# Performance work log

Hardware: AMD Instinct MI355X
Metric: run time of the kernel (lower is better)

Reference implementation:

```python
import jax, jax.numpy as jnp
import numpy as np

B, T, C = 2, 2048, 2048
H, KV = 16, 4
D = C // H            # 128 head dim
G = H // KV           # 4 query heads per kv head
THETA = 10000.0


def setup_inputs() -> dict:
    key = jax.random.key(0)
    k0, k1, k2, k3 = jax.random.split(key, 4)
    s = 1.0 / np.sqrt(C)
    return {
        "x": jax.random.normal(k0, (B, T, C), jnp.float32),
        "Wq": jax.random.normal(k1, (H * D, C), jnp.float32) * s,
        "Wkv": jax.random.normal(k2, (2 * KV * D, C), jnp.float32) * s,
        "Wo": jax.random.normal(k3, (C, C), jnp.float32) * s,
    }


def _rotate_half(x):
    d = x.shape[-1] // 2
    return jnp.concatenate([-x[..., d:], x[..., :d]], axis=-1)


def _rope_tables(t, d):
    freqs = 1.0 / (THETA ** (jnp.arange(0, d, 2, dtype=jnp.float32) / d))
    ang = jnp.arange(t, dtype=jnp.float32)[:, None] * freqs[None, :]  # [T, d/2]
    emb = jnp.concatenate([ang, ang], axis=-1)                         # [T, d]
    return jnp.cos(emb), jnp.sin(emb)


def reference(x, Wq, Wkv, Wo):
    b, t, c = x.shape
    q = (x @ Wq.T).reshape(b, t, H, D).transpose(0, 2, 1, 3)      # [B,H,T,D]
    kv = (x @ Wkv.T).reshape(b, t, 2 * KV, D)
    k = kv[:, :, :KV].transpose(0, 2, 1, 3)                        # [B,KV,T,D]
    v = kv[:, :, KV:].transpose(0, 2, 1, 3)                        # [B,KV,T,D]

    cos, sin = _rope_tables(t, D)
    cos, sin = cos[None, None], sin[None, None]                    # [1,1,T,D]
    q = q * cos + _rotate_half(q) * sin
    k = k * cos + _rotate_half(k) * sin

    # GQA: keep k/v at KV heads; reshape q into [B,KV,G,T,D] instead of expanding k/v.
    qg = q.reshape(b, KV, G, t, D)
    scores = jnp.einsum('bkgtd,bksd->bkgts', qg, k) / jnp.sqrt(jnp.float32(D))
    causal = jnp.tril(jnp.ones((t, t), dtype=bool))                # is_causal=True path
    scores = jnp.where(causal, scores, -jnp.inf)
    p = jax.nn.softmax(scores, axis=-1)
    y = jnp.einsum('bkgts,bksd->bkgtd', p, v)                      # [B,KV,G,T,D]
    y = y.reshape(b, H, t, D).transpose(0, 2, 1, 3).reshape(b, t, c)
    return y @ Wo.T
```

## Files before the change

### kernel.cpp

```cpp
#include <hip/hip_runtime.h>

typedef unsigned short u16;
typedef __attribute__((ext_vector_type(4))) float f32x4;
typedef __attribute__((ext_vector_type(8))) __bf16 bf16x8;

__device__ __forceinline__ u16 f2bf(float f) {
    unsigned int x = __float_as_uint(f);
    x += 0x7fffu + ((x >> 16) & 1u);
    return (u16)(x >> 16);
}
__device__ __forceinline__ float bf2f(u16 u) {
    return __uint_as_float(((unsigned int)u) << 16);
}
__device__ __forceinline__ void async16(const void* g, void* l) {
    __builtin_amdgcn_global_load_lds(
        (const __attribute__((address_space(1))) void*)g,
        (__attribute__((address_space(3))) void*)l,
        16, 0, 0);
}
__device__ __forceinline__ void barrier_fence() {
    asm volatile("" ::: "memory");
    __builtin_amdgcn_s_barrier();
    asm volatile("" ::: "memory");
}

__global__ __launch_bounds__(256)
void cvt_all(const float* __restrict__ x,  const float* __restrict__ wq,
             const float* __restrict__ wkv, const float* __restrict__ wo,
             u16* __restrict__ xb, u16* __restrict__ wqb,
             u16* __restrict__ wkvb, u16* __restrict__ wob)
{
    const int nx = 8388608, nq = 4194304, nkv = 2097152;
    const int i = (blockIdx.x * 256 + threadIdx.x) * 4;
    const float* src; u16* dst; int off;
    if (i < nx)                 { src = x;   dst = xb;   off = i; }
    else if (i < nx + nq)       { src = wq;  dst = wqb;  off = i - nx; }
    else if (i < nx + nq + nkv) { src = wkv; dst = wkvb; off = i - nx - nq; }
    else                        { src = wo;  dst = wob;  off = i - nx - nq - nkv; }
    const float4 v = *(const float4*)(src + off);
    ushort4 o;
    o.x = f2bf(v.x); o.y = f2bf(v.y); o.z = f2bf(v.z); o.w = f2bf(v.w);
    *(ushort4*)(dst + off) = o;
}

__global__ __launch_bounds__(256, 3)
void gemm_qkv(const u16* __restrict__ A,
              const u16* __restrict__ B0,
              const u16* __restrict__ B1,
              u16* __restrict__ C,
              u16* __restrict__ vbuf,
              int M, int K)
{
    constexpr int ASZ = 128 * 32;
    __shared__ __align__(16) u16 As[3 * ASZ];
    __shared__ __align__(16) u16 Bs[3 * ASZ];

    const int tid  = threadIdx.x;
    const int w    = tid >> 6;
    const int lane = tid & 63;
    const int fl   = lane & 15;
    const int q4   = lane >> 4;
    const int wm   = w >> 1;
    const int wn   = w & 1;

    const int gx  = gridDim.x;
    const int nwg = gx * gridDim.y;
    int id = blockIdx.y * gx + blockIdx.x;
    id = (id & 7) * (nwg >> 3) + (id >> 3);
    const int m0 = (id / gx) * 128;
    const int n0 = (id % gx) * 128;

    const u16* Bp = B0;
    int nb = n0;
    if (n0 >= 2048) { Bp = B1; nb = n0 - 2048; }

    const int srow = w * 16 + (lane >> 2);
    const int sg   = (lane & 3) ^ ((lane >> 3) & 3);
    const u16* agp = A  + (size_t)(m0 + srow) * K + sg * 8;
    const u16* bgp = Bp + (size_t)(nb + srow) * K + sg * 8;
    const int sLds = w * 512;

    const int cSlot = (q4 ^ ((fl >> 1) & 3)) * 8;

    f32x4 acc[4][4];
    #pragma unroll
    for (int i = 0; i < 4; ++i)
        #pragma unroll
        for (int j = 0; j < 4; ++j)
            acc[i][j] = f32x4{0.f, 0.f, 0.f, 0.f};

    const int NT = K >> 5;

    auto stage = [&](int t, int bf) {
        const size_t kof = (size_t)t * 32;
        async16(agp + kof,                   &As[bf * ASZ + sLds]);
        async16(agp + (size_t)64 * K + kof,  &As[bf * ASZ + 2048 + sLds]);
        async16(bgp + kof,                   &Bs[bf * ASZ + sLds]);
        async16(bgp + (size_t)64 * K + kof,  &Bs[bf * ASZ + 2048 + sLds]);
    };

    stage(0, 0);
    stage(1, 1);

    int bf = 0;
    for (int t = 0; t < NT; ++t) {
        if (t < NT - 1) asm volatile("s_waitcnt vmcnt(4)" ::: "memory");
        else            asm volatile("s_waitcnt vmcnt(0)" ::: "memory");
        barrier_fence();
        const int bf2 = (bf + 2 >= 3) ? bf - 1 : bf + 2;
        if (t + 2 < NT) stage(t + 2, bf2);

        const int ab = bf * ASZ + (wm * 64 + fl) * 32 + cSlot;
        const int bb = bf * ASZ + (wn * 32 + fl) * 32 + cSlot;
        bf16x8 a[4], b[4];
        #pragma unroll
        for (int mt = 0; mt < 4; ++mt)
            a[mt] = *(const bf16x8*)&As[ab + mt * 512];
        b[0] = *(const bf16x8*)&Bs[bb];
        b[1] = *(const bf16x8*)&Bs[bb + 512];
        b[2] = *(const bf16x8*)&Bs[bb + 2048];
        b[3] = *(const bf16x8*)&Bs[bb + 2560];

        #pragma unroll
        for (int mt = 0; mt < 4; ++mt)
            #pragma unroll
            for (int nt = 0; nt < 4; ++nt)
                acc[mt][nt] = __builtin_amdgcn_mfma_f32_16x16x32_bf16(
                    a[mt], b[nt], acc[mt][nt], 0, 0, 0);

        bf = (bf + 1 >= 3) ? 0 : bf + 1;
    }

    if (n0 < 2560) {
        const float sc = (n0 < 2048) ? 0.08838834764831845f : 1.0f;
        float inv[2];
        #pragma unroll
        for (int j = 0; j < 2; ++j)
            inv[j] = exp2f(-(float)(wn * 32 + j * 16 + fl) * 0.2076205f);
        #pragma unroll
        for (int mt = 0; mt < 4; ++mt) {
            #pragma unroll
            for (int r = 0; r < 4; ++r) {
                const int row = m0 + wm * 64 + mt * 16 + q4 * 4 + r;
                const float pos = (float)(row & 2047);
                #pragma unroll
                for (int j = 0; j < 2; ++j) {
                    float s, c;
                    __sincosf(pos * inv[j], &s, &c);
                    const float x1 = acc[mt][j][r];
                    const float x2 = acc[mt][j + 2][r];
                    const int i0 = wn * 32 + j * 16 + fl;
                    C[(size_t)row * 3072 + n0 + i0]      = f2bf((x1 * c - x2 * s) * sc);
                    C[(size_t)row * 3072 + n0 + 64 + i0] = f2bf((x2 * c + x1 * s) * sc);
                }
            }
        }
    } else {
        #pragma unroll
        for (int mt = 0; mt < 4; ++mt)
            #pragma unroll
            for (int j = 0; j < 4; ++j) {
                const int colb = n0 + wn * 32 + (j & 1) * 16 + (j >> 1) * 64 + fl;
                const int f = colb - 2560;
                #pragma unroll
                for (int r = 0; r < 4; ++r) {
                    const int row = m0 + wm * 64 + mt * 16 + q4 * 4 + r;
                    const int tt = row & 2047;
                    const int bb2 = row >> 11;
                    vbuf[((size_t)((bb2 << 2) + (f >> 7)) * 128 + (f & 127)) * 2048 + tt] =
                        f2bf(acc[mt][j][r]);
                }
            }
    }
}

__global__ __launch_bounds__(256, 3)
void gemm128r(const u16* __restrict__ A,
              const u16* __restrict__ B0,
              float* __restrict__ Cf,
              int M, int N, int K)
{
    constexpr int ASZ = 128 * 32;
    __shared__ __align__(16) u16 As[3 * ASZ];
    __shared__ __align__(16) u16 Bs[3 * ASZ];

    const int tid  = threadIdx.x;
    const int w    = tid >> 6;
    const int lane = tid & 63;
    const int fl   = lane & 15;
    const int q4   = lane >> 4;
    const int wm   = w >> 1;
    const int wn   = w & 1;

    const int gx  = gridDim.x;
    const int nwg = gx * gridDim.y;
    int id = blockIdx.y * gx + blockIdx.x;
    id = (id & 7) * (nwg >> 3) + (id >> 3);
    const int m0 = (id / gx) * 128;
    const int n0 = (id % gx) * 128;

    const int srow = w * 16 + (lane >> 2);
    const int sg   = (lane & 3) ^ ((lane >> 3) & 3);
    const u16* agp = A  + (size_t)(m0 + srow) * K + sg * 8;
    const u16* bgp = B0 + (size_t)(n0 + srow) * K + sg * 8;
    const int sLds = w * 512;

    const int cSlot = (q4 ^ ((fl >> 1) & 3)) * 8;

    f32x4 acc[4][4];
    #pragma unroll
    for (int i = 0; i < 4; ++i)
        #pragma unroll
        for (int j = 0; j < 4; ++j)
            acc[i][j] = f32x4{0.f, 0.f, 0.f, 0.f};

    const int NT = K >> 5;

    auto stage = [&](int t, int bf) {
        const size_t kof = (size_t)t * 32;
        async16(agp + kof,                   &As[bf * ASZ + sLds]);
        async16(agp + (size_t)64 * K + kof,  &As[bf * ASZ + 2048 + sLds]);
        async16(bgp + kof,                   &Bs[bf * ASZ + sLds]);
        async16(bgp + (size_t)64 * K + kof,  &Bs[bf * ASZ + 2048 + sLds]);
    };

    stage(0, 0);
    stage(1, 1);

    int bf = 0;
    for (int t = 0; t < NT; ++t) {
        if (t < NT - 1) asm volatile("s_waitcnt vmcnt(4)" ::: "memory");
        else            asm volatile("s_waitcnt vmcnt(0)" ::: "memory");
        barrier_fence();
        const int bf2 = (bf + 2 >= 3) ? bf - 1 : bf + 2;
        if (t + 2 < NT) stage(t + 2, bf2);

        const int ab = bf * ASZ + (wm * 64 + fl) * 32 + cSlot;
        const int bb = bf * ASZ + (wn * 64 + fl) * 32 + cSlot;
        bf16x8 a[4], b[4];
        #pragma unroll
        for (int mt = 0; mt < 4; ++mt)
            a[mt] = *(const bf16x8*)&As[ab + mt * 512];
        #pragma unroll
        for (int nt = 0; nt < 4; ++nt)
            b[nt] = *(const bf16x8*)&Bs[bb + nt * 512];

        #pragma unroll
        for (int mt = 0; mt < 4; ++mt)
            #pragma unroll
            for (int nt = 0; nt < 4; ++nt)
                acc[mt][nt] = __builtin_amdgcn_mfma_f32_16x16x32_bf16(
                    a[mt], b[nt], acc[mt][nt], 0, 0, 0);

        bf = (bf + 1 >= 3) ? 0 : bf + 1;
    }

    #pragma unroll
    for (int mt = 0; mt < 4; ++mt)
        #pragma unroll
        for (int nt = 0; nt < 4; ++nt) {
            const int colb = n0 + wn * 64 + nt * 16 + fl;
            #pragma unroll
            for (int r = 0; r < 4; ++r) {
                const int row = m0 + wm * 64 + mt * 16 + q4 * 4 + r;
                Cf[(size_t)row * N + colb] = acc[mt][nt][r];
            }
        }
}

__global__ __launch_bounds__(256, 2)
void attn_kernel(const u16* __restrict__ qkv,
                 const u16* __restrict__ vsrc,
                 u16* __restrict__ y)
{
    constexpr int T = 2048;
    const int lo  = blockIdx.x;
    const int hi  = 31 - lo;
    const int bh  = blockIdx.y;
    const int b   = bh >> 4;
    const int h   = bh & 15;
    const int kvh = h >> 2;

    const int tid  = threadIdx.x;
    const int w    = tid >> 6;
    const int lane = tid & 63;
    const int fl   = lane & 15;
    const int q4   = lane >> 4;

    __shared__ __align__(16) u16 Ks[2][64 * 128];
    __shared__ __align__(16) u16 Vt[2][128 * 64];
    __shared__ __align__(16) u16 Ps[64 * 72];

    const u16* Qg = qkv  + (size_t)(b * T) * 3072 + (h << 7);
    const u16* Kg = qkv  + (size_t)(b * T) * 3072 + 2048 + (kvh << 7);
    const u16* Vg = vsrc + (size_t)((b * 4 + kvh) * 128) * T;

    bf16x8 qf0[4], qf1[4];
    #pragma unroll
    for (int kc = 0; kc < 4; ++kc) {
        qf0[kc] = *(const bf16x8*)&Qg[(size_t)(lo * 64 + w * 16 + fl) * 3072 + kc * 32 + q4 * 8];
        qf1[kc] = *(const bf16x8*)&Qg[(size_t)(hi * 64 + w * 16 + fl) * 3072 + kc * 32 + q4 * 8];
    }

    int goffK[4], goffV[4], ldsC[4];
    #pragma unroll
    for (int i = 0; i < 4; ++i) {
        const int c  = w + 4 * i;
        const int rk = 4 * c + (lane >> 4);
        const int lk = (lane & 15) ^ (rk & 15);
        goffK[i] = rk * 3072 + lk * 8;
        const int rv = 8 * c + (lane >> 3);
        const int lv = (lane & 7) ^ ((lane >> 3) & 7);
        goffV[i] = rv * T + lv * 8;
        ldsC[i]  = c * 512;
    }

    #pragma unroll
    for (int i = 0; i < 4; ++i) {
        async16(Kg + goffK[i], &Ks[0][ldsC[i]]);
        async16(Vg + goffV[i], &Vt[0][ldsC[i]]);
    }

    float l0 = 0.f, l1 = 0.f;
    f32x4 o0[8], o1[8];
    #pragma unroll
    for (int dt = 0; dt < 8; ++dt) {
        o0[dt] = f32x4{0.f, 0.f, 0.f, 0.f};
        o1[dt] = f32x4{0.f, 0.f, 0.f, 0.f};
    }

    const int psrow = (w * 16 + fl) * 72;

    for (int j = 0; j <= hi; ++j) {
        __syncthreads();

        if (j < hi) {
            const u16* kb = Kg + (size_t)(j + 1) * 64 * 3072;
            const u16* vb = Vg + (j + 1) * 64;
            const int nb = (j + 1) & 1;
            #pragma unroll
            for (int i = 0; i < 4; ++i) {
                async16(kb + goffK[i], &Ks[nb][ldsC[i]]);
                async16(vb + goffV[i], &Vt[nb][ldsC[i]]);
            }
        }
        const int cb = j & 1;
        const bool dual = (j <= lo);

        f32x4 s0[4], s1[4];
        #pragma unroll
        for (int nt = 0; nt < 4; ++nt) {
            s0[nt] = f32x4{0.f, 0.f, 0.f, 0.f};
            s1[nt] = f32x4{0.f, 0.f, 0.f, 0.f};
        }
        if (dual) {
            #pragma unroll
            for (int kc = 0; kc < 4; ++kc)
                #pragma unroll
                for (int nt = 0; nt < 4; ++nt) {
                    bf16x8 aK = *(const bf16x8*)
                        &Ks[cb][(nt * 16 + fl) * 128 + (((kc << 2) + q4) ^ fl) * 8];
                    s1[nt] = __builtin_amdgcn_mfma_f32_16x16x32_bf16(aK, qf1[kc], s1[nt], 0, 0, 0);
                    s0[nt] = __builtin_amdgcn_mfma_f32_16x16x32_bf16(aK, qf0[kc], s0[nt], 0, 0, 0);
                }
        } else {
            #pragma unroll
            for (int kc = 0; kc < 4; ++kc)
                #pragma unroll
                for (int nt = 0; nt < 4; ++nt) {
                    bf16x8 aK = *(const bf16x8*)
                        &Ks[cb][(nt * 16 + fl) * 128 + (((kc << 2) + q4) ^ fl) * 8];
                    s1[nt] = __builtin_amdgcn_mfma_f32_16x16x32_bf16(aK, qf1[kc], s1[nt], 0, 0, 0);
                }
        }

        if (j == lo || j == hi) {
            const int qloc = w * 16 + fl;
            #pragma unroll
            for (int nt = 0; nt < 4; ++nt)
                #pragma unroll
                for (int r = 0; r < 4; ++r)
                    if (nt * 16 + q4 * 4 + r > qloc) {
                        if (j == lo) s0[nt][r] = -3e38f;
                        else         s1[nt][r] = -3e38f;
                    }
        }

        if (dual) {
            #pragma unroll
            for (int nt = 0; nt < 4; ++nt) {
                ushort4 pw;
                float p0 = __expf(s0[nt][0]);
                float p1 = __expf(s0[nt][1]);
                float p2 = __expf(s0[nt][2]);
                float p3 = __expf(s0[nt][3]);
                l0 += (p0 + p1) + (p2 + p3);
                pw.x = f2bf(p0); pw.y = f2bf(p1); pw.z = f2bf(p2); pw.w = f2bf(p3);
                *(ushort4*)&Ps[psrow + nt * 16 + q4 * 4] = pw;
            }
            asm volatile("s_waitcnt lgkmcnt(0)" ::: "memory");
            #pragma unroll
            for (int kc = 0; kc < 2; ++kc) {
                bf16x8 ap = *(const bf16x8*)&Ps[psrow + kc * 32 + q4 * 8];
                #pragma unroll
                for (int dt = 0; dt < 8; ++dt) {
                    bf16x8 bv = *(const bf16x8*)
                        &Vt[cb][(dt * 16 + fl) * 64 + (((kc << 2) + q4) ^ (fl & 7)) * 8];
                    o0[dt] = __builtin_amdgcn_mfma_f32_16x16x32_bf16(ap, bv, o0[dt], 0, 0, 0);
                }
            }
        }

        #pragma unroll
        for (int nt = 0; nt < 4; ++nt) {
            ushort4 pw;
            float p0 = __expf(s1[nt][0]);
            float p1 = __expf(s1[nt][1]);
            float p2 = __expf(s1[nt][2]);
            float p3 = __expf(s1[nt][3]);
            l1 += (p0 + p1) + (p2 + p3);
            pw.x = f2bf(p0); pw.y = f2bf(p1); pw.z = f2bf(p2); pw.w = f2bf(p3);
            *(ushort4*)&Ps[psrow + nt * 16 + q4 * 4] = pw;
        }
        asm volatile("s_waitcnt lgkmcnt(0)" ::: "memory");
        #pragma unroll
        for (int kc = 0; kc < 2; ++kc) {
            bf16x8 ap = *(const bf16x8*)&Ps[psrow + kc * 32 + q4 * 8];
            #pragma unroll
            for (int dt = 0; dt < 8; ++dt) {
                bf16x8 bv = *(const bf16x8*)
                    &Vt[cb][(dt * 16 + fl) * 64 + (((kc << 2) + q4) ^ (fl & 7)) * 8];
                o1[dt] = __builtin_amdgcn_mfma_f32_16x16x32_bf16(ap, bv, o1[dt], 0, 0, 0);
            }
        }
    }

    l0 += __shfl_xor(l0, 16, 64);
    l0 += __shfl_xor(l0, 32, 64);
    l1 += __shfl_xor(l1, 16, 64);
    l1 += __shfl_xor(l1, 32, 64);
    const float li0 = 1.0f / l0;
    const float li1 = 1.0f / l1;

    float lr0[4], lr1[4];
    #pragma unroll
    for (int r = 0; r < 4; ++r) {
        lr0[r] = __shfl(li0, q4 * 4 + r, 16);
        lr1[r] = __shfl(li1, q4 * 4 + r, 16);
    }
    #pragma unroll
    for (int dt = 0; dt < 8; ++dt)
        #pragma unroll
        for (int r = 0; r < 4; ++r) {
            const int row0 = lo * 64 + w * 16 + q4 * 4 + r;
            const int row1 = hi * 64 + w * 16 + q4 * 4 + r;
            y[(size_t)(b * T + row0) * 2048 + (h << 7) + dt * 16 + fl] =
                f2bf(o0[dt][r] * lr0[r]);
            y[(size_t)(b * T + row1) * 2048 + (h << 7) + dt * 16 + fl] =
                f2bf(o1[dt][r] * lr1[r]);
        }
}

extern "C" void kernel_launch(void* const* d_in, const int* in_sizes, int n_in,
                              void* d_out, int out_size, void* d_ws, size_t ws_size,
                              hipStream_t stream)
{
    const float* x   = (const float*)d_in[0];
    const float* Wq  = (const float*)d_in[1];
    const float* Wkv = (const float*)d_in[2];
    const float* Wo  = (const float*)d_in[3];
    float* out = (float*)d_out;

    const int nx = 4096 * 2048, nq = 2048 * 2048, nkv = 1024 * 2048, no = 2048 * 2048;

    u16* xb   = (u16*)d_ws;
    u16* wqb  = xb  + nx;
    u16* wkvb = wqb + nq;
    u16* wob  = wkvb + nkv;
    u16* qkv  = wob + no;
    u16* vbuf = qkv + (size_t)4096 * 3072;
    u16* y    = vbuf + (size_t)2 * 4 * 128 * 2048;

    const int ntot = nx + nq + nkv + no;
    cvt_all<<<ntot / 1024, 256, 0, stream>>>(x, Wq, Wkv, Wo, xb, wqb, wkvb, wob);

    dim3 g1(3072 / 128, 4096 / 128);
    gemm_qkv<<<g1, 256, 0, stream>>>(xb, wqb, wkvb, qkv, vbuf, 4096, 2048);

    attn_kernel<<<dim3(16, 32), 256, 0, stream>>>(qkv, vbuf, y);

    dim3 g2(2048 / 128, 4096 / 128);
    gemm128r<<<g2, 256, 0, stream>>>(y, wob, out, 4096, 2048, 2048);
}
```

Before: 273.3 us.

## Rework attention around 32x32 MFMA with register-resident P

```diff
diff --git a/kernel.cpp b/kernel.cpp
--- a/kernel.cpp
+++ b/kernel.cpp
@@ -2,6 +2,7 @@
 
 typedef unsigned short u16;
 typedef __attribute__((ext_vector_type(4))) float f32x4;
+typedef __attribute__((ext_vector_type(16))) float f32x16;
 typedef __attribute__((ext_vector_type(8))) __bf16 bf16x8;
 
 __device__ __forceinline__ u16 f2bf(float f) {
@@ -22,6 +23,11 @@
     asm volatile("" ::: "memory");
     __builtin_amdgcn_s_barrier();
     asm volatile("" ::: "memory");
+}
+__device__ __forceinline__ unsigned cvtpk(float lo, float hi) {
+    unsigned d;
+    asm("v_cvt_pk_bf16_f32 %0, %1, %2" : "=v"(d) : "v"(lo), "v"(hi));
+    return d;
 }
 
 __global__ __launch_bounds__(256)
@@ -274,191 +280,135 @@
                  u16* __restrict__ y)
 {
     constexpr int T = 2048;
-    const int lo  = blockIdx.x;
-    const int hi  = 31 - lo;
-    const int bh  = blockIdx.y;
-    const int b   = bh >> 4;
-    const int h   = bh & 15;
-    const int kvh = h >> 2;
+    const int bh = blockIdx.x;
+    const int by = blockIdx.y;
+    const int qt = (by < 8) ? by : 23 - by;
+    const int b = bh >> 4, h = bh & 15, kvh = h >> 2;
 
     const int tid  = threadIdx.x;
     const int w    = tid >> 6;
     const int lane = tid & 63;
-    const int fl   = lane & 15;
-    const int q4   = lane >> 4;
-
-    __shared__ __align__(16) u16 Ks[2][64 * 128];
-    __shared__ __align__(16) u16 Vt[2][128 * 64];
-    __shared__ __align__(16) u16 Ps[64 * 72];
+    const int l31  = lane & 31;
+    const int hh   = lane >> 5;
+
+    __shared__ __align__(16) u16 Ks[2][32 * 128];
+    __shared__ __align__(16) u16 Vt[2][128 * 32];
 
     const u16* Qg = qkv  + (size_t)(b * T) * 3072 + (h << 7);
     const u16* Kg = qkv  + (size_t)(b * T) * 3072 + 2048 + (kvh << 7);
     const u16* Vg = vsrc + (size_t)((b * 4 + kvh) * 128) * T;
 
-    bf16x8 qf0[4], qf1[4];
-    #pragma unroll
-    for (int kc = 0; kc < 4; ++kc) {
-        qf0[kc] = *(const bf16x8*)&Qg[(size_t)(lo * 64 + w * 16 + fl) * 3072 + kc * 32 + q4 * 8];
-        qf1[kc] = *(const bf16x8*)&Qg[(size_t)(hi * 64 + w * 16 + fl) * 3072 + kc * 32 + q4 * 8];
-    }
-
-    int goffK[4], goffV[4], ldsC[4];
-    #pragma unroll
-    for (int i = 0; i < 4; ++i) {
+    const int qb = qt * 128 + w * 32;
+    bf16x8 qf[8];
+    #pragma unroll
+    for (int kc = 0; kc < 8; ++kc)
+        qf[kc] = *(const bf16x8*)&Qg[(size_t)(qb + l31) * 3072 + kc * 16 + hh * 8];
+
+    int goffK[2], goffV[2], ldsC[2];
+    #pragma unroll
+    for (int i = 0; i < 2; ++i) {
         const int c  = w + 4 * i;
         const int rk = 4 * c + (lane >> 4);
         const int lk = (lane & 15) ^ (rk & 15);
         goffK[i] = rk * 3072 + lk * 8;
-        const int rv = 8 * c + (lane >> 3);
-        const int lv = (lane & 7) ^ ((lane >> 3) & 7);
+        const int rv = 16 * c + (lane >> 2);
+        const int lv = (lane & 3) ^ ((lane >> 3) & 3);
         goffV[i] = rv * T + lv * 8;
         ldsC[i]  = c * 512;
     }
 
     #pragma unroll
-    for (int i = 0; i < 4; ++i) {
+    for (int i = 0; i < 2; ++i) {
         async16(Kg + goffK[i], &Ks[0][ldsC[i]]);
         async16(Vg + goffV[i], &Vt[0][ldsC[i]]);
     }
 
-    float l0 = 0.f, l1 = 0.f;
-    f32x4 o0[8], o1[8];
-    #pragma unroll
-    for (int dt = 0; dt < 8; ++dt) {
-        o0[dt] = f32x4{0.f, 0.f, 0.f, 0.f};
-        o1[dt] = f32x4{0.f, 0.f, 0.f, 0.f};
-    }
-
-    const int psrow = (w * 16 + fl) * 72;
-
-    for (int j = 0; j <= hi; ++j) {
+    f32x16 o[4];
+    #pragma unroll
+    for (int dt = 0; dt < 4; ++dt)
+        #pragma unroll
+        for (int r = 0; r < 16; ++r)
+            o[dt][r] = 0.f;
+    float lsum = 0.f;
+
+    const int NJ = 4 * qt + 4;
+    const int jw = 4 * qt + w;
+    const int aswz = l31 & 15;
+    const int vswz = (l31 >> 1) & 3;
+
+    for (int j = 0; j < NJ; ++j) {
         __syncthreads();
 
-        if (j < hi) {
-            const u16* kb = Kg + (size_t)(j + 1) * 64 * 3072;
-            const u16* vb = Vg + (j + 1) * 64;
+        if (j + 1 < NJ) {
+            const u16* kb = Kg + (size_t)(j + 1) * 32 * 3072;
+            const u16* vb = Vg + (j + 1) * 32;
             const int nb = (j + 1) & 1;
             #pragma unroll
-            for (int i = 0; i < 4; ++i) {
+            for (int i = 0; i < 2; ++i) {
                 async16(kb + goffK[i], &Ks[nb][ldsC[i]]);
                 async16(vb + goffV[i], &Vt[nb][ldsC[i]]);
             }
         }
         const int cb = j & 1;
-        const bool dual = (j <= lo);
-
-        f32x4 s0[4], s1[4];
-        #pragma unroll
-        for (int nt = 0; nt < 4; ++nt) {
-            s0[nt] = f32x4{0.f, 0.f, 0.f, 0.f};
-            s1[nt] = f32x4{0.f, 0.f, 0.f, 0.f};
-        }
-        if (dual) {
-            #pragma unroll
-            for (int kc = 0; kc < 4; ++kc)
-                #pragma unroll
-                for (int nt = 0; nt < 4; ++nt) {
-                    bf16x8 aK = *(const bf16x8*)
-                        &Ks[cb][(nt * 16 + fl) * 128 + (((kc << 2) + q4) ^ fl) * 8];
-                    s1[nt] = __builtin_amdgcn_mfma_f32_16x16x32_bf16(aK, qf1[kc], s1[nt], 0, 0, 0);
-                    s0[nt] = __builtin_amdgcn_mfma_f32_16x16x32_bf16(aK, qf0[kc], s0[nt], 0, 0, 0);
-                }
-        } else {
-            #pragma unroll
-            for (int kc = 0; kc < 4; ++kc)
-                #pragma unroll
-                for (int nt = 0; nt < 4; ++nt) {
-                    bf16x8 aK = *(const bf16x8*)
-                        &Ks[cb][(nt * 16 + fl) * 128 + (((kc << 2) + q4) ^ fl) * 8];
-                    s1[nt] = __builtin_amdgcn_mfma_f32_16x16x32_bf16(aK, qf1[kc], s1[nt], 0, 0, 0);
-                }
-        }
-
-        if (j == lo || j == hi) {
-            const int qloc = w * 16 + fl;
-            #pragma unroll
-            for (int nt = 0; nt < 4; ++nt)
-                #pragma unroll
-                for (int r = 0; r < 4; ++r)
-                    if (nt * 16 + q4 * 4 + r > qloc) {
-                        if (j == lo) s0[nt][r] = -3e38f;
-                        else         s1[nt][r] = -3e38f;
-                    }
-        }
-
-        if (dual) {
-            #pragma unroll
-            for (int nt = 0; nt < 4; ++nt) {
-                ushort4 pw;
-                float p0 = __expf(s0[nt][0]);
-                float p1 = __expf(s0[nt][1]);
-                float p2 = __expf(s0[nt][2]);
-                float p3 = __expf(s0[nt][3]);
-                l0 += (p0 + p1) + (p2 + p3);
-                pw.x = f2bf(p0); pw.y = f2bf(p1); pw.z = f2bf(p2); pw.w = f2bf(p3);
-                *(ushort4*)&Ps[psrow + nt * 16 + q4 * 4] = pw;
-            }
-            asm volatile("s_waitcnt lgkmcnt(0)" ::: "memory");
-            #pragma unroll
-            for (int kc = 0; kc < 2; ++kc) {
-                bf16x8 ap = *(const bf16x8*)&Ps[psrow + kc * 32 + q4 * 8];
-                #pragma unroll
-                for (int dt = 0; dt < 8; ++dt) {
-                    bf16x8 bv = *(const bf16x8*)
-                        &Vt[cb][(dt * 16 + fl) * 64 + (((kc << 2) + q4) ^ (fl & 7)) * 8];
-                    o0[dt] = __builtin_amdgcn_mfma_f32_16x16x32_bf16(ap, bv, o0[dt], 0, 0, 0);
-                }
-            }
-        }
-
-        #pragma unroll
-        for (int nt = 0; nt < 4; ++nt) {
-            ushort4 pw;
-            float p0 = __expf(s1[nt][0]);
-            float p1 = __expf(s1[nt][1]);
-            float p2 = __expf(s1[nt][2]);
-            float p3 = __expf(s1[nt][3]);
-            l1 += (p0 + p1) + (p2 + p3);
-            pw.x = f2bf(p0); pw.y = f2bf(p1); pw.z = f2bf(p2); pw.w = f2bf(p3);
-            *(ushort4*)&Ps[psrow + nt * 16 + q4 * 4] = pw;
-        }
-        asm volatile("s_waitcnt lgkmcnt(0)" ::: "memory");
+        if (j > jw) continue;
+
+        f32x16 s;
+        #pragma unroll
+        for (int r = 0; r < 16; ++r) s[r] = 0.f;
+        #pragma unroll
+        for (int kc = 0; kc < 8; ++kc) {
+            bf16x8 aK = *(const bf16x8*)
+                &Ks[cb][l31 * 128 + ((2 * kc + hh) ^ aswz) * 8];
+            s = __builtin_amdgcn_mfma_f32_32x32x16_bf16(aK, qf[kc], s, 0, 0, 0);
+        }
+
+        if (j == jw) {
+            #pragma unroll
+            for (int r = 0; r < 16; ++r) {
+                const int kvl = (r & 3) + 8 * (r >> 2) + 4 * hh;
+                if (kvl > l31) s[r] = -3e38f;
+            }
+        }
+
+        float p[16];
+        #pragma unroll
+        for (int r = 0; r < 16; ++r) {
+            p[r] = __expf(s[r]);
+            lsum += p[r];
+        }
+
         #pragma unroll
         for (int kc = 0; kc < 2; ++kc) {
-            bf16x8 ap = *(const bf16x8*)&Ps[psrow + kc * 32 + q4 * 8];
-            #pragma unroll
-            for (int dt = 0; dt < 8; ++dt) {
+            unsigned A0 = cvtpk(p[8 * kc + 0], p[8 * kc + 1]);
+            unsigned A1 = cvtpk(p[8 * kc + 2], p[8 * kc + 3]);
+            unsigned B0 = cvtpk(p[8 * kc + 4], p[8 * kc + 5]);
+            unsigned B1 = cvtpk(p[8 * kc + 6], p[8 * kc + 7]);
+            asm volatile("v_permlane32_swap_b32 %0, %1" : "+v"(A0), "+v"(B0));
+            asm volatile("v_permlane32_swap_b32 %0, %1" : "+v"(A1), "+v"(B1));
+            union { unsigned u[4]; bf16x8 v; } pu;
+            pu.u[0] = A0; pu.u[1] = A1; pu.u[2] = B0; pu.u[3] = B1;
+            const bf16x8 pa = pu.v;
+            #pragma unroll
+            for (int dt = 0; dt < 4; ++dt) {
                 bf16x8 bv = *(const bf16x8*)
-                    &Vt[cb][(dt * 16 + fl) * 64 + (((kc << 2) + q4) ^ (fl & 7)) * 8];
-                o1[dt] = __builtin_amdgcn_mfma_f32_16x16x32_bf16(ap, bv, o1[dt], 0, 0, 0);
-            }
-        }
-    }
-
-    l0 += __shfl_xor(l0, 16, 64);
-    l0 += __shfl_xor(l0, 32, 64);
-    l1 += __shfl_xor(l1, 16, 64);
-    l1 += __shfl_xor(l1, 32, 64);
-    const float li0 = 1.0f / l0;
-    const float li1 = 1.0f / l1;
-
-    float lr0[4], lr1[4];
-    #pragma unroll
-    for (int r = 0; r < 4; ++r) {
-        lr0[r] = __shfl(li0, q4 * 4 + r, 16);
-        lr1[r] = __shfl(li1, q4 * 4 + r, 16);
-    }
-    #pragma unroll
-    for (int dt = 0; dt < 8; ++dt)
-        #pragma unroll
-        for (int r = 0; r < 4; ++r) {
-            const int row0 = lo * 64 + w * 16 + q4 * 4 + r;
-            const int row1 = hi * 64 + w * 16 + q4 * 4 + r;
-            y[(size_t)(b * T + row0) * 2048 + (h << 7) + dt * 16 + fl] =
-                f2bf(o0[dt][r] * lr0[r]);
-            y[(size_t)(b * T + row1) * 2048 + (h << 7) + dt * 16 + fl] =
-                f2bf(o1[dt][r] * lr1[r]);
-        }
+                    &Vt[cb][(dt * 32 + l31) * 32 + ((2 * kc + hh) ^ vswz) * 8];
+                o[dt] = __builtin_amdgcn_mfma_f32_32x32x16_bf16(pa, bv, o[dt], 0, 0, 0);
+            }
+        }
+    }
+
+    lsum += __shfl_xor(lsum, 32, 64);
+    const float linv = 1.0f / lsum;
+
+    #pragma unroll
+    for (int r = 0; r < 16; ++r) {
+        const int qloc = (r & 3) + 8 * (r >> 2) + 4 * hh;
+        const float lr = __shfl(linv, qloc, 64);
+        const size_t row = (size_t)(b * T + qb + qloc);
+        #pragma unroll
+        for (int dt = 0; dt < 4; ++dt)
+            y[row * 2048 + (h << 7) + dt * 32 + l31] = f2bf(o[dt][r] * lr);
+    }
 }
 
 extern "C" void kernel_launch(void* const* d_in, const int* in_sizes, int n_in,
@@ -487,7 +437,7 @@
     dim3 g1(3072 / 128, 4096 / 128);
     gemm_qkv<<<g1, 256, 0, stream>>>(xb, wqb, wkvb, qkv, vbuf, 4096, 2048);
 
-    attn_kernel<<<dim3(16, 32), 256, 0, stream>>>(qkv, vbuf, y);
+    attn_kernel<<<dim3(32, 16), 256, 0, stream>>>(qkv, vbuf, y);
 
     dim3 g2(2048 / 128, 4096 / 128);
     gemm128r<<<g2, 256, 0, stream>>>(y, wob, out, 4096, 2048, 2048);
```

After: 289.5 us. 5.9% more time.

## Fuse fp32-to-bf16 conversion into QKV GEMM loads and drop standalone convert pass

Applied to the files above, without the earlier changes.

```diff
diff --git a/kernel.cpp b/kernel.cpp
--- a/kernel.cpp
+++ b/kernel.cpp
@@ -23,151 +23,172 @@
     __builtin_amdgcn_s_barrier();
     asm volatile("" ::: "memory");
 }
-
-__global__ __launch_bounds__(256)
-void cvt_all(const float* __restrict__ x,  const float* __restrict__ wq,
-             const float* __restrict__ wkv, const float* __restrict__ wo,
-             u16* __restrict__ xb, u16* __restrict__ wqb,
-             u16* __restrict__ wkvb, u16* __restrict__ wob)
+__device__ __forceinline__ unsigned cvtpk(float lo, float hi) {
+    unsigned d;
+    asm("v_cvt_pk_bf16_f32 %0, %1, %2" : "=v"(d) : "v"(lo), "v"(hi));
+    return d;
+}
+
+__global__ __launch_bounds__(512, 4)
+void gemm_qkv_f32(const float* __restrict__ A,
+                  const float* __restrict__ B0,
+                  const float* __restrict__ B1,
+                  const float* __restrict__ wo,
+                  u16* __restrict__ wob,
+                  u16* __restrict__ C,
+                  u16* __restrict__ vbuf,
+                  int M, int K)
 {
-    const int nx = 8388608, nq = 4194304, nkv = 2097152;
-    const int i = (blockIdx.x * 256 + threadIdx.x) * 4;
-    const float* src; u16* dst; int off;
-    if (i < nx)                 { src = x;   dst = xb;   off = i; }
-    else if (i < nx + nq)       { src = wq;  dst = wqb;  off = i - nx; }
-    else if (i < nx + nq + nkv) { src = wkv; dst = wkvb; off = i - nx - nq; }
-    else                        { src = wo;  dst = wob;  off = i - nx - nq - nkv; }
-    const float4 v = *(const float4*)(src + off);
-    ushort4 o;
-    o.x = f2bf(v.x); o.y = f2bf(v.y); o.z = f2bf(v.z); o.w = f2bf(v.w);
-    *(ushort4*)(dst + off) = o;
-}
-
-__global__ __launch_bounds__(256, 3)
-void gemm_qkv(const u16* __restrict__ A,
-              const u16* __restrict__ B0,
-              const u16* __restrict__ B1,
-              u16* __restrict__ C,
-              u16* __restrict__ vbuf,
-              int M, int K)
-{
-    constexpr int ASZ = 128 * 32;
-    __shared__ __align__(16) u16 As[3 * ASZ];
-    __shared__ __align__(16) u16 Bs[3 * ASZ];
-
-    const int tid  = threadIdx.x;
+    const int raw = blockIdx.x;
+    const int tid = threadIdx.x;
+
+    if (raw >= 768) {
+        int idx = (raw - 768) * 512 + tid;
+        #pragma unroll 4
+        for (int p = 0; p < 32; ++p) {
+            const int i = (idx + p * 32768) * 4;
+            const float4 v = *(const float4*)(wo + i);
+            ushort4 o;
+            o.x = f2bf(v.x); o.y = f2bf(v.y); o.z = f2bf(v.z); o.w = f2bf(v.w);
+            *(ushort4*)(wob + i) = o;
+        }
+        return;
+    }
+
+    __shared__ __align__(16) u16 As[2][4096];
+    __shared__ __align__(16) u16 Bs[2][4096];
+
     const int w    = tid >> 6;
     const int lane = tid & 63;
     const int fl   = lane & 15;
     const int q4   = lane >> 4;
-    const int wm   = w >> 1;
-    const int wn   = w & 1;
-
-    const int gx  = gridDim.x;
-    const int nwg = gx * gridDim.y;
-    int id = blockIdx.y * gx + blockIdx.x;
-    id = (id & 7) * (nwg >> 3) + (id >> 3);
-    const int m0 = (id / gx) * 128;
-    const int n0 = (id % gx) * 128;
-
-    const u16* Bp = B0;
+    const int wm   = w >> 2;
+    const int wn   = w & 3;
+
+    int id = (raw & 7) * 96 + (raw >> 3);
+    const int m0 = (id / 24) * 128;
+    const int n0 = (id % 24) * 128;
+
+    const float* Bp = B0;
     int nb = n0;
     if (n0 >= 2048) { Bp = B1; nb = n0 - 2048; }
 
-    const int srow = w * 16 + (lane >> 2);
-    const int sg   = (lane & 3) ^ ((lane >> 3) & 3);
-    const u16* agp = A  + (size_t)(m0 + srow) * K + sg * 8;
-    const u16* bgp = Bp + (size_t)(nb + srow) * K + sg * 8;
-    const int sLds = w * 512;
+    const int wq   = w & 3;
+    const int srow = wq * 32 + (lane >> 1);
+    const int ch   = lane & 1;
+    const bool isA = (w < 4);
+    const float* sp = isA ? (A + (size_t)(m0 + srow) * K + ch * 16)
+                          : (Bp + (size_t)(nb + srow) * K + ch * 16);
+    u16* sl = isA ? &As[0][0] : &Bs[0][0];
+    const int f_   = (lane >> 2) & 3;
+    const int s0   = (2 * ch) ^ f_;
+    const int s1   = (2 * ch + 1) ^ f_;
+    const int wbase = srow * 32;
 
     const int cSlot = (q4 ^ ((fl >> 1) & 3)) * 8;
-
-    f32x4 acc[4][4];
-    #pragma unroll
-    for (int i = 0; i < 4; ++i)
-        #pragma unroll
-        for (int j = 0; j < 4; ++j)
-            acc[i][j] = f32x4{0.f, 0.f, 0.f, 0.f};
+    const int aBase = (wm * 64 + fl) * 32 + cSlot;
+    const int bBase0 = (wn * 16 + fl) * 32 + cSlot;
+    const int bBase1 = (64 + wn * 16 + fl) * 32 + cSlot;
+
+    f32x4 acc[4][2];
+    #pragma unroll
+    for (int i = 0; i < 4; ++i) {
+        acc[i][0] = f32x4{0.f, 0.f, 0.f, 0.f};
+        acc[i][1] = f32x4{0.f, 0.f, 0.f, 0.f};
+    }
 
     const int NT = K >> 5;
-
-    auto stage = [&](int t, int bf) {
-        const size_t kof = (size_t)t * 32;
-        async16(agp + kof,                   &As[bf * ASZ + sLds]);
-        async16(agp + (size_t)64 * K + kof,  &As[bf * ASZ + 2048 + sLds]);
-        async16(bgp + kof,                   &Bs[bf * ASZ + sLds]);
-        async16(bgp + (size_t)64 * K + kof,  &Bs[bf * ASZ + 2048 + sLds]);
+    float4 L[4];
+
+    auto issueLoads = [&](int t) {
+        const float* p = sp + (size_t)t * 32;
+        L[0] = *(const float4*)(p);
+        L[1] = *(const float4*)(p + 4);
+        L[2] = *(const float4*)(p + 8);
+        L[3] = *(const float4*)(p + 12);
     };
 
-    stage(0, 0);
-    stage(1, 1);
-
-    int bf = 0;
+    issueLoads(0);
+    {
+        unsigned g[8];
+        g[0] = cvtpk(L[0].x, L[0].y); g[1] = cvtpk(L[0].z, L[0].w);
+        g[2] = cvtpk(L[1].x, L[1].y); g[3] = cvtpk(L[1].z, L[1].w);
+        g[4] = cvtpk(L[2].x, L[2].y); g[5] = cvtpk(L[2].z, L[2].w);
+        g[6] = cvtpk(L[3].x, L[3].y); g[7] = cvtpk(L[3].z, L[3].w);
+        unsigned* d0 = (unsigned*)(sl + wbase + s0 * 8);
+        unsigned* d1 = (unsigned*)(sl + wbase + s1 * 8);
+        d0[0] = g[0]; d0[1] = g[1]; d0[2] = g[2]; d0[3] = g[3];
+        d1[0] = g[4]; d1[1] = g[5]; d1[2] = g[6]; d1[3] = g[7];
+    }
+    issueLoads(1);
+
     for (int t = 0; t < NT; ++t) {
-        if (t < NT - 1) asm volatile("s_waitcnt vmcnt(4)" ::: "memory");
-        else            asm volatile("s_waitcnt vmcnt(0)" ::: "memory");
+        const int bf = t & 1;
+        asm volatile("s_waitcnt lgkmcnt(0)" ::: "memory");
         barrier_fence();
-        const int bf2 = (bf + 2 >= 3) ? bf - 1 : bf + 2;
-        if (t + 2 < NT) stage(t + 2, bf2);
-
-        const int ab = bf * ASZ + (wm * 64 + fl) * 32 + cSlot;
-        const int bb = bf * ASZ + (wn * 32 + fl) * 32 + cSlot;
-        bf16x8 a[4], b[4];
+
+        bf16x8 a[4], b[2];
         #pragma unroll
         for (int mt = 0; mt < 4; ++mt)
-            a[mt] = *(const bf16x8*)&As[ab + mt * 512];
-        b[0] = *(const bf16x8*)&Bs[bb];
-        b[1] = *(const bf16x8*)&Bs[bb + 512];
-        b[2] = *(const bf16x8*)&Bs[bb + 2048];
-        b[3] = *(const bf16x8*)&Bs[bb + 2560];
-
-        #pragma unroll
-        for (int mt = 0; mt < 4; ++mt)
-            #pragma unroll
-            for (int nt = 0; nt < 4; ++nt)
-                acc[mt][nt] = __builtin_amdgcn_mfma_f32_16x16x32_bf16(
-                    a[mt], b[nt], acc[mt][nt], 0, 0, 0);
-
-        bf = (bf + 1 >= 3) ? 0 : bf + 1;
+            a[mt] = *(const bf16x8*)&As[bf][aBase + mt * 512];
+        b[0] = *(const bf16x8*)&Bs[bf][bBase0];
+        b[1] = *(const bf16x8*)&Bs[bf][bBase1];
+
+        #pragma unroll
+        for (int mt = 0; mt < 4; ++mt) {
+            acc[mt][0] = __builtin_amdgcn_mfma_f32_16x16x32_bf16(
+                a[mt], b[0], acc[mt][0], 0, 0, 0);
+            acc[mt][1] = __builtin_amdgcn_mfma_f32_16x16x32_bf16(
+                a[mt], b[1], acc[mt][1], 0, 0, 0);
+        }
+
+        if (t + 1 < NT) {
+            asm volatile("s_waitcnt vmcnt(0)" ::: "memory");
+            unsigned g[8];
+            g[0] = cvtpk(L[0].x, L[0].y); g[1] = cvtpk(L[0].z, L[0].w);
+            g[2] = cvtpk(L[1].x, L[1].y); g[3] = cvtpk(L[1].z, L[1].w);
+            g[4] = cvtpk(L[2].x, L[2].y); g[5] = cvtpk(L[2].z, L[2].w);
+            g[6] = cvtpk(L[3].x, L[3].y); g[7] = cvtpk(L[3].z, L[3].w);
+            u16* base = sl + ((t + 1) & 1) * 4096 + wbase;
+            unsigned* d0 = (unsigned*)(base + s0 * 8);
+            unsigned* d1 = (unsigned*)(base + s1 * 8);
+            d0[0] = g[0]; d0[1] = g[1]; d0[2] = g[2]; d0[3] = g[3];
+            d1[0] = g[4]; d1[1] = g[5]; d1[2] = g[6]; d1[3] = g[7];
+            if (t + 2 < NT) issueLoads(t + 2);
+        }
     }
 
     if (n0 < 2560) {
         const float sc = (n0 < 2048) ? 0.08838834764831845f : 1.0f;
-        float inv[2];
-        #pragma unroll
-        for (int j = 0; j < 2; ++j)
-            inv[j] = exp2f(-(float)(wn * 32 + j * 16 + fl) * 0.2076205f);
+        const int i0 = wn * 16 + fl;
+        const float inv = exp2f(-(float)i0 * 0.2076205f);
         #pragma unroll
         for (int mt = 0; mt < 4; ++mt) {
             #pragma unroll
             for (int r = 0; r < 4; ++r) {
                 const int row = m0 + wm * 64 + mt * 16 + q4 * 4 + r;
                 const float pos = (float)(row & 2047);
-                #pragma unroll
-                for (int j = 0; j < 2; ++j) {
-                    float s, c;
-                    __sincosf(pos * inv[j], &s, &c);
-                    const float x1 = acc[mt][j][r];
-                    const float x2 = acc[mt][j + 2][r];
-                    const int i0 = wn * 32 + j * 16 + fl;
-                    C[(size_t)row * 3072 + n0 + i0]      = f2bf((x1 * c - x2 * s) * sc);
-                    C[(size_t)row * 3072 + n0 + 64 + i0] = f2bf((x2 * c + x1 * s) * sc);
-                }
+                float s, c;
+                __sincosf(pos * inv, &s, &c);
+                const float x1 = acc[mt][0][r];
+                const float x2 = acc[mt][1][r];
+                C[(size_t)row * 3072 + n0 + i0]      = f2bf((x1 * c - x2 * s) * sc);
+                C[(size_t)row * 3072 + n0 + 64 + i0] = f2bf((x2 * c + x1 * s) * sc);
             }
         }
     } else {
         #pragma unroll
         for (int mt = 0; mt < 4; ++mt)
             #pragma unroll
-            for (int j = 0; j < 4; ++j) {
-                const int colb = n0 + wn * 32 + (j & 1) * 16 + (j >> 1) * 64 + fl;
-                const int f = colb - 2560;
+            for (int j = 0; j < 2; ++j) {
+                const int colb = n0 + j * 64 + wn * 16 + fl;
+                const int fc = colb - 2560;
                 #pragma unroll
                 for (int r = 0; r < 4; ++r) {
                     const int row = m0 + wm * 64 + mt * 16 + q4 * 4 + r;
                     const int tt = row & 2047;
                     const int bb2 = row >> 11;
-                    vbuf[((size_t)((bb2 << 2) + (f >> 7)) * 128 + (f & 127)) * 2048 + tt] =
+                    vbuf[((size_t)((bb2 << 2) + (fc >> 7)) * 128 + (fc & 127)) * 2048 + tt] =
                         f2bf(acc[mt][j][r]);
                 }
             }
@@ -471,21 +492,12 @@
     const float* Wo  = (const float*)d_in[3];
     float* out = (float*)d_out;
 
-    const int nx = 4096 * 2048, nq = 2048 * 2048, nkv = 1024 * 2048, no = 2048 * 2048;
-
-    u16* xb   = (u16*)d_ws;
-    u16* wqb  = xb  + nx;
-    u16* wkvb = wqb + nq;
-    u16* wob  = wkvb + nkv;
-    u16* qkv  = wob + no;
+    u16* wob  = (u16*)d_ws;
+    u16* qkv  = wob + (size_t)2048 * 2048;
     u16* vbuf = qkv + (size_t)4096 * 3072;
     u16* y    = vbuf + (size_t)2 * 4 * 128 * 2048;
 
-    const int ntot = nx + nq + nkv + no;
-    cvt_all<<<ntot / 1024, 256, 0, stream>>>(x, Wq, Wkv, Wo, xb, wqb, wkvb, wob);
-
-    dim3 g1(3072 / 128, 4096 / 128);
-    gemm_qkv<<<g1, 256, 0, stream>>>(xb, wqb, wkvb, qkv, vbuf, 4096, 2048);
+    gemm_qkv_f32<<<832, 512, 0, stream>>>(x, Wq, Wkv, Wo, wob, qkv, vbuf, 4096, 2048);
 
     attn_kernel<<<dim3(16, 32), 256, 0, stream>>>(qkv, vbuf, y);
 
```

After: 322.9 us. +18.1%, slower.
